# Kernel optimization log

Measured on AMD Instinct MI355X. Metric: run time of the kernel, lower is better.

## Reference

```python
import jax, jax.numpy as jnp
import numpy as np

EMB = 768
HEADS = 8
HEAD_DIM = EMB // HEADS
SCALE = HEAD_DIM ** -0.5


def setup_inputs() -> dict:
    key = jax.random.key(0)
    ks = jax.random.split(key, 9)
    s = EMB ** -0.5
    return {
        "x": jax.random.normal(ks[0], (2, 4096, EMB), dtype=jnp.float32),
        "Wq": jax.random.normal(ks[1], (EMB, EMB), dtype=jnp.float32) * s,
        "bq": jax.random.normal(ks[2], (EMB,), dtype=jnp.float32) * 0.02,
        "Wk": jax.random.normal(ks[3], (EMB, EMB), dtype=jnp.float32) * s,
        "bk": jax.random.normal(ks[4], (EMB,), dtype=jnp.float32) * 0.02,
        "Wv": jax.random.normal(ks[5], (EMB, EMB), dtype=jnp.float32) * s,
        "bv": jax.random.normal(ks[6], (EMB,), dtype=jnp.float32) * 0.02,
        "Wo": jax.random.normal(ks[7], (EMB, EMB), dtype=jnp.float32) * s,
        "bo": jax.random.normal(ks[8], (EMB,), dtype=jnp.float32) * 0.02,
    }


def reference(x, Wq, bq, Wk, bk, Wv, bv, Wo, bo):
    b, n, _ = x.shape
    def split_heads(t):  # [b, n, emb] -> [b, h, n, d]
        return t.reshape(b, n, HEADS, HEAD_DIM).transpose(0, 2, 1, 3)
    q = split_heads(x @ Wq + bq)
    k = split_heads(x @ Wk + bk)
    v = split_heads(x @ Wv + bv)
    scores = jnp.einsum('bhqd,bhkd->bhqk', q, k)
    # NOTE: faithful to source — softmax first, THEN multiply by scale.
    attn = jax.nn.softmax(scores, axis=-1) * SCALE
    out = jnp.einsum('bhqk,bhkd->bhqd', attn, v)
    out = out.transpose(0, 2, 1, 3).reshape(b, n, EMB)
    return out @ Wo + bo
```

## Files before the change

kernel.cpp:

```cpp
#include <hip/hip_runtime.h>
#include <hip/hip_fp16.h>


typedef _Float16 half8 __attribute__((ext_vector_type(8)));
typedef _Float16 half4 __attribute__((ext_vector_type(4)));
typedef float   float4_ __attribute__((ext_vector_type(4)));
typedef float   f32x16 __attribute__((ext_vector_type(16)));

#define SCALE 0.102062072615966f
#define LOG2E 1.44269504088896340736f

__device__ __forceinline__ float4_ mfma16(half8 a, half8 b, float4_ c) {
    return __builtin_amdgcn_mfma_f32_16x16x32_f16(a, b, c, 0, 0, 0);
}
__device__ __forceinline__ f32x16 mfma32(half8 a, half8 b, f32x16 c) {
    return __builtin_amdgcn_mfma_f32_32x32x16_f16(a, b, c, 0, 0, 0);
}
__device__ __forceinline__ void gload16(const _Float16* g, _Float16* l) {
    __builtin_amdgcn_global_load_lds(
        (const __attribute__((address_space(1))) void*)g,
        (__attribute__((address_space(3))) void*)l, 16, 0, 0);
}


__global__ void cast_x(const float* __restrict__ x, _Float16* __restrict__ xb) {
    int i = blockIdx.x * 256 + threadIdx.x;
    float4_ v = ((const float4_*)x)[i];
    half4 h = { (_Float16)v[0], (_Float16)v[1], (_Float16)v[2], (_Float16)v[3] };
    ((half4*)xb)[i] = h;
}

__global__ void prep_w(const float* __restrict__ Wq, const float* __restrict__ Wk,
                       const float* __restrict__ Wv, const float* __restrict__ Wo,
                       _Float16* __restrict__ wqkv, _Float16* __restrict__ wot) {
    __shared__ float tile[64][65];
    const int bid = blockIdx.x;
    const int mat = bid / 144, rem = bid % 144;
    const int kt = rem / 12, ct = rem % 12;
    const float* W = (mat == 0) ? Wq : (mat == 1) ? Wk : (mat == 2) ? Wv : Wo;
    const int k0 = kt * 64, c0 = ct * 64;
    const int t = threadIdx.x;
    const int lr = t >> 4, lc = (t & 15) * 4;
    #pragma unroll
    for (int i = 0; i < 4; ++i) {
        float4_ v = *(const float4_*)(W + (size_t)(k0 + i * 16 + lr) * 768 + c0 + lc);
        tile[i * 16 + lr][lc + 0] = v[0];
        tile[i * 16 + lr][lc + 1] = v[1];
        tile[i * 16 + lr][lc + 2] = v[2];
        tile[i * 16 + lr][lc + 3] = v[3];
    }
    __syncthreads();
    const int cr = t >> 2, kq = (t & 3) * 16;
    _Float16* dst = (mat < 3) ? (wqkv + ((size_t)(mat * 768 + c0 + cr)) * 768 + k0 + kq)
                              : (wot  + ((size_t)(c0 + cr)) * 768 + k0 + kq);
    half8 h0, h1;
    #pragma unroll
    for (int j = 0; j < 8; ++j) {
        h0[j] = (_Float16)tile[kq + j][cr];
        h1[j] = (_Float16)tile[kq + 8 + j][cr];
    }
    *(half8*)dst = h0;
    *(half8*)(dst + 8) = h1;
}

__global__ void prep_bias(const float* __restrict__ bq, const float* __restrict__ bk,
                          const float* __restrict__ bv, float* __restrict__ bqkv) {
    int i = blockIdx.x * 256 + threadIdx.x;
    float v = (i < 768) ? bq[i] : (i < 1536) ? bk[i - 768] : bv[i - 1536];
    bqkv[i] = v;
}

__global__ __launch_bounds__(256, 2) void gemm_kernel(
    const _Float16* __restrict__ A, const _Float16* __restrict__ Bt,
    const float* __restrict__ bias, int mode,
    _Float16* __restrict__ Qo, _Float16* __restrict__ Ko, _Float16* __restrict__ Vto,
    float* __restrict__ out)
{
    __shared__ alignas(16) _Float16 Af[16 * 512];
    __shared__ alignas(16) _Float16 Bf[16 * 512];
    const int tid = threadIdx.x;
    const int lane = tid & 63, w = tid >> 6;
    const int wm = w >> 1, wn = w & 1;
    const int l15 = lane & 15, l4 = lane >> 4;
    const int m0 = blockIdx.y * 128;
    const int n0 = blockIdx.x * 128;

    const _Float16* gs[8];
    _Float16* ld[8];
    #pragma unroll
    for (int i = 0; i < 8; ++i) {
        int f = (w & 1) * 8 + i;
        int rg = f >> 1, kc = f & 1;
        int r0 = ((w < 2) ? m0 : n0) + rg * 16;
        gs[i] = ((w < 2) ? A : Bt) + (size_t)(r0 + l15) * 768 + kc * 32 + l4 * 8;
        ld[i] = ((w < 2) ? Af : Bf) + f * 512;
    }

    float4_ acc[4][4] = {};

    for (int k0 = 0; k0 < 768; k0 += 64) {
        #pragma unroll
        for (int i = 0; i < 8; ++i)
            gload16(gs[i] + k0, ld[i]);
        __syncthreads();
        #pragma unroll
        for (int kc = 0; kc < 2; ++kc) {
            half8 bfr[4];
            #pragma unroll
            for (int nt = 0; nt < 4; ++nt)
                bfr[nt] = *(const half8*)(Bf + (size_t)(((wn * 4 + nt) * 2 + kc) * 512 + lane * 8));
            #pragma unroll
            for (int mt = 0; mt < 4; ++mt) {
                half8 afr = *(const half8*)(Af + (size_t)(((wm * 4 + mt) * 2 + kc) * 512 + lane * 8));
                #pragma unroll
                for (int nt = 0; nt < 4; ++nt)
                    acc[mt][nt] = mfma16(afr, bfr[nt], acc[mt][nt]);
            }
        }
        __syncthreads();
    }

    #pragma unroll
    for (int mt = 0; mt < 4; ++mt)
    #pragma unroll
    for (int nt = 0; nt < 4; ++nt) {
        int gc = n0 + wn * 64 + nt * 16 + l15;
        float bv_ = bias[gc];
        #pragma unroll
        for (int r = 0; r < 4; ++r) {
            int gm = m0 + wm * 64 + mt * 16 + l4 * 4 + r;
            float val = acc[mt][nt][r] + bv_;
            if (mode == 1) {
                out[(size_t)gm * 768 + gc] = val;
            } else {
                int b = gm >> 12, n = gm & 4095;
                if (gc < 768) {
                    int h = gc / 96, d = gc % 96;
                    Qo[(((size_t)(b * 8 + h)) * 4096 + n) * 96 + d] = (_Float16)(val * LOG2E);
                } else if (gc < 1536) {
                    int c = gc - 768, h = c / 96, d = c % 96;
                    int bh = b * 8 + h;
                    size_t idx = (((size_t)bh * 128 + (n >> 5)) * 6 + (d >> 4)) * 512
                               + (size_t)((d >> 3) & 1) * 256 + (size_t)(n & 31) * 8 + (d & 7);
                    Ko[idx] = (_Float16)val;
                } else {
                    int c = gc - 1536, h = c / 96, d = c % 96;
                    int bh = b * 8 + h;
                    size_t idx = (((size_t)bh * 64 + (n >> 6)) * 12 + ((n >> 4) & 3) * 3 + (d >> 5)) * 512
                               + (size_t)((n >> 3) & 1) * 256 + (size_t)(d & 31) * 8 + (n & 7);
                    Vto[idx] = (_Float16)val;
                }
            }
        }
    }
}

__global__ __launch_bounds__(256, 2) void attn_kernel(
    const _Float16* __restrict__ Q, const _Float16* __restrict__ Kf,
    const _Float16* __restrict__ Vf, _Float16* __restrict__ AO)
{
    __shared__ alignas(16) _Float16 kvbuf[2][24 * 512];
    __shared__ float tab[4][32];

    const int tid = threadIdx.x;
    const int lane = tid & 63, w = tid >> 6;
    const int l31 = lane & 31, hi = lane >> 5;

    const int B = blockIdx.x;
    const int xcd = B & 7, j = B >> 3;
    const int bh = 2 * xcd + (j >> 5);
    const int qb = j & 31;
    const int q0 = qb * 128 + w * 32;

    const size_t qBase = (size_t)bh * 4096 * 96;
    const _Float16* kfb = Kf + (size_t)bh * 393216;
    const _Float16* vfb = Vf + (size_t)bh * 393216;

    half8 qf[6];
    #pragma unroll
    for (int dch = 0; dch < 6; ++dch)
        qf[dch] = *(const half8*)(Q + qBase + (size_t)(q0 + l31) * 96 + dch * 16 + hi * 8);

    f32x16 o0 = {}, o1 = {}, o2 = {};
    float m = -1e30f, l = 0.f;

    const int fbase = w * 6;
    const _Float16* gbase = ((fbase < 12) ? (kfb + (size_t)fbase * 512)
                                          : (vfb + (size_t)(fbase - 12) * 512)) + lane * 8;

    #pragma unroll
    for (int i = 0; i < 6; ++i)
        gload16(gbase + i * 512, &kvbuf[0][(fbase + i) * 512]);
    __syncthreads();

    int cur = 0;
    for (int t = 0; t < 64; ++t) {
        const int tn = (t + 1) & 63;
        #pragma unroll
        for (int i = 0; i < 6; ++i)
            gload16(gbase + (size_t)tn * 6144 + i * 512, &kvbuf[cur ^ 1][(fbase + i) * 512]);

        const _Float16* kb = &kvbuf[cur][0];
        const _Float16* vb = &kvbuf[cur][12 * 512];

        f32x16 s0 = {}, s1 = {};
        __builtin_amdgcn_s_setprio(1);
        #pragma unroll
        for (int dch = 0; dch < 6; ++dch) {
            half8 k0 = *(const half8*)(kb + dch * 512 + lane * 8);
            half8 k1 = *(const half8*)(kb + (6 + dch) * 512 + lane * 8);
            s0 = mfma32(k0, qf[dch], s0);
            s1 = mfma32(k1, qf[dch], s1);
        }
        __builtin_amdgcn_s_setprio(0);

        float lm = fmaxf(s0[0], s0[1]);
        #pragma unroll
        for (int r = 2; r < 16; ++r) lm = fmaxf(lm, s0[r]);
        #pragma unroll
        for (int r = 0; r < 16; ++r) lm = fmaxf(lm, s1[r]);
        float pmax = fmaxf(lm, __shfl_xor(lm, 32));
        if (__any(pmax > m + 8.0f)) {
            float mn = fmaxf(m, pmax);
            float al = __builtin_exp2f(m - mn);
            m = mn; l *= al;
            if (hi == 0) tab[w][l31] = al;
            asm volatile("s_waitcnt lgkmcnt(0)" ::: "memory");
            #pragma unroll
            for (int r = 0; r < 16; ++r) {
                float alr = tab[w][(r & 3) + 8 * (r >> 2) + 4 * hi];
                o0[r] *= alr; o1[r] *= alr; o2[r] *= alr;
            }
        }
        float ls = 0.f;
        uint32_t Lp[16];
        #pragma unroll
        for (int kg = 0; kg < 2; ++kg) {
            const f32x16& s = kg ? s1 : s0;
            #pragma unroll
            for (int jg = 0; jg < 4; ++jg) {
                float p0 = __builtin_exp2f(s[4 * jg + 0] - m);
                float p1 = __builtin_exp2f(s[4 * jg + 1] - m);
                float p2 = __builtin_exp2f(s[4 * jg + 2] - m);
                float p3 = __builtin_exp2f(s[4 * jg + 3] - m);
                ls += (p0 + p1) + (p2 + p3);
                union { _Float16 h[2]; uint32_t u; } pk0, pk1;
                pk0.h[0] = (_Float16)p0; pk0.h[1] = (_Float16)p1;
                pk1.h[0] = (_Float16)p2; pk1.h[1] = (_Float16)p3;
                Lp[kg * 8 + jg * 2] = pk0.u; Lp[kg * 8 + jg * 2 + 1] = pk1.u;
            }
        }
        l += ls + __shfl_xor(ls, 32);

        half8 pa[4];
        #pragma unroll
        for (int kk = 0; kk < 4; ++kk) {
            uint32_t u0 = Lp[4 * kk], u1 = Lp[4 * kk + 1];
            uint32_t u2 = Lp[4 * kk + 2], u3 = Lp[4 * kk + 3];
            asm("v_permlane32_swap_b32 %0, %1" : "+v"(u0), "+v"(u2));
            asm("v_permlane32_swap_b32 %0, %1" : "+v"(u1), "+v"(u3));
            union { half8 h; uint32_t u[4]; } fr;
            fr.u[0] = u0; fr.u[1] = u1; fr.u[2] = u2; fr.u[3] = u3;
            pa[kk] = fr.h;
        }

        __builtin_amdgcn_s_setprio(1);
        #pragma unroll
        for (int kk = 0; kk < 4; ++kk) {
            half8 v0 = *(const half8*)(vb + (kk * 3 + 0) * 512 + lane * 8);
            half8 v1 = *(const half8*)(vb + (kk * 3 + 1) * 512 + lane * 8);
            half8 v2 = *(const half8*)(vb + (kk * 3 + 2) * 512 + lane * 8);
            o0 = mfma32(pa[kk], v0, o0);
            o1 = mfma32(pa[kk], v1, o1);
            o2 = mfma32(pa[kk], v2, o2);
        }
        __builtin_amdgcn_s_setprio(0);

        __syncthreads();
        cur ^= 1;
    }

    if (hi == 0) tab[w][l31] = l;
    asm volatile("s_waitcnt lgkmcnt(0)" ::: "memory");
    const int b = bh >> 3, h = bh & 7;
    #pragma unroll
    for (int r = 0; r < 16; ++r) {
        int qrow = (r & 3) + 8 * (r >> 2) + 4 * hi;
        float inv = SCALE / tab[w][qrow];
        int n = q0 + qrow;
        size_t base = ((size_t)(b * 4096 + n)) * 768 + h * 96 + l31;
        AO[base]      = (_Float16)(o0[r] * inv);
        AO[base + 32] = (_Float16)(o1[r] * inv);
        AO[base + 64] = (_Float16)(o2[r] * inv);
    }
}


extern "C" void kernel_launch(void* const* d_in, const int* in_sizes, int n_in,
                              void* d_out, int out_size, void* d_ws, size_t ws_size,
                              hipStream_t stream) {
    const float* x  = (const float*)d_in[0];
    const float* Wq = (const float*)d_in[1];
    const float* bq = (const float*)d_in[2];
    const float* Wk = (const float*)d_in[3];
    const float* bk = (const float*)d_in[4];
    const float* Wv = (const float*)d_in[5];
    const float* bv = (const float*)d_in[6];
    const float* Wo = (const float*)d_in[7];
    const float* bo = (const float*)d_in[8];
    float* out = (float*)d_out;

    char* ws = (char*)d_ws;
    _Float16* xb   = (_Float16*)(ws);
    _Float16* wqkv = (_Float16*)(ws + 12582912);
    _Float16* wot  = (_Float16*)(ws + 16121856);
    float*    bqkv = (float*)   (ws + 17301504);
    _Float16* Qb   = (_Float16*)(ws + 17310720);
    _Float16* Kfb  = (_Float16*)(ws + 29893632);
    _Float16* Vfb  = (_Float16*)(ws + 42476544);
    _Float16* AO   = xb;

    cast_x<<<6144, 256, 0, stream>>>(x, xb);
    prep_w<<<576, 256, 0, stream>>>(Wq, Wk, Wv, Wo, wqkv, wot);
    prep_bias<<<9, 256, 0, stream>>>(bq, bk, bv, bqkv);

    gemm_kernel<<<dim3(18, 64), 256, 0, stream>>>(xb, wqkv, bqkv, 0, Qb, Kfb, Vfb, nullptr);

    attn_kernel<<<512, 256, 0, stream>>>(Qb, Kfb, Vfb, AO);

    gemm_kernel<<<dim3(6, 64), 256, 0, stream>>>(AO, wot, bo, 1, nullptr, nullptr, nullptr, out);
}
```

Measured before the change: 280.2 us.

## Stage K/V tiles through registers instead of direct global-to-LDS loads

Replaces the asynchronous global_load_lds prefetch with ordinary global loads into registers, which are written to the other LDS buffer after the PV matmul, behind an extra barrier. It also replaces the permlane32 swaps with shfl_xor plus selects, restructures the row-max reduction into a tree, and lowers the rescale threshold from 8 to 6. The register staging adds 24 VGPRs, a second __syncthreads per tile and extra LDS store instructions. The shuffle path is likely more costly than the native permlane swap.

```diff
diff --git a/kernel.cpp b/kernel.cpp
--- a/kernel.cpp
+++ b/kernel.cpp
@@ -159,7 +159,7 @@
     const _Float16* __restrict__ Q, const _Float16* __restrict__ Kf,
     const _Float16* __restrict__ Vf, _Float16* __restrict__ AO)
 {
-    __shared__ alignas(16) _Float16 kvbuf[2][24 * 512];
+    __shared__ alignas(16) _Float16 lds[2][24 * 512];
     __shared__ float tab[4][32];
 
     const int tid = threadIdx.x;
@@ -185,45 +185,58 @@
     float m = -1e30f, l = 0.f;
 
     const int fbase = w * 6;
-    const _Float16* gbase = ((fbase < 12) ? (kfb + (size_t)fbase * 512)
-                                          : (vfb + (size_t)(fbase - 12) * 512)) + lane * 8;
-
+    half8 streg[6];
+
+    #pragma unroll
+    for (int i = 0; i < 6; ++i) {
+        int f = fbase + i;
+        const _Float16* g = (f < 12 ? kfb + (size_t)f * 512
+                                    : vfb + (size_t)(f - 12) * 512) + lane * 8;
+        streg[i] = *(const half8*)g;
+    }
     #pragma unroll
     for (int i = 0; i < 6; ++i)
-        gload16(gbase + i * 512, &kvbuf[0][(fbase + i) * 512]);
+        *(half8*)(&lds[0][(fbase + i) * 512 + lane * 8]) = streg[i];
     __syncthreads();
 
     int cur = 0;
     for (int t = 0; t < 64; ++t) {
         const int tn = (t + 1) & 63;
         #pragma unroll
-        for (int i = 0; i < 6; ++i)
-            gload16(gbase + (size_t)tn * 6144 + i * 512, &kvbuf[cur ^ 1][(fbase + i) * 512]);
-
-        const _Float16* kb = &kvbuf[cur][0];
-        const _Float16* vb = &kvbuf[cur][12 * 512];
+        for (int i = 0; i < 6; ++i) {
+            int f = fbase + i;
+            const _Float16* g = (f < 12 ? kfb + ((size_t)tn * 12 + f) * 512
+                                        : vfb + ((size_t)tn * 12 + (f - 12)) * 512) + lane * 8;
+            streg[i] = *(const half8*)g;
+        }
+
+        const _Float16* kb = &lds[cur][0];
+        const _Float16* vb = &lds[cur][12 * 512];
 
         f32x16 s0 = {}, s1 = {};
         __builtin_amdgcn_s_setprio(1);
         #pragma unroll
         for (int dch = 0; dch < 6; ++dch) {
-            half8 k0 = *(const half8*)(kb + dch * 512 + lane * 8);
-            half8 k1 = *(const half8*)(kb + (6 + dch) * 512 + lane * 8);
+            half8 k0 = *(const half8*)(kb + (0 * 6 + dch) * 512 + lane * 8);
+            half8 k1 = *(const half8*)(kb + (1 * 6 + dch) * 512 + lane * 8);
             s0 = mfma32(k0, qf[dch], s0);
             s1 = mfma32(k1, qf[dch], s1);
         }
         __builtin_amdgcn_s_setprio(0);
 
-        float lm = fmaxf(s0[0], s0[1]);
-        #pragma unroll
-        for (int r = 2; r < 16; ++r) lm = fmaxf(lm, s0[r]);
-        #pragma unroll
-        for (int r = 0; r < 16; ++r) lm = fmaxf(lm, s1[r]);
+        float mx[8];
+        #pragma unroll
+        for (int r = 0; r < 8; ++r)
+            mx[r] = fmaxf(fmaxf(s0[r], s0[r + 8]), fmaxf(s1[r], s1[r + 8]));
+        mx[0] = fmaxf(mx[0], mx[4]); mx[1] = fmaxf(mx[1], mx[5]);
+        mx[2] = fmaxf(mx[2], mx[6]); mx[3] = fmaxf(mx[3], mx[7]);
+        float lm = fmaxf(fmaxf(mx[0], mx[1]), fmaxf(mx[2], mx[3]));
         float pmax = fmaxf(lm, __shfl_xor(lm, 32));
-        if (__any(pmax > m + 8.0f)) {
+        if (__any(pmax > m + 6.0f)) {
             float mn = fmaxf(m, pmax);
             float al = __builtin_exp2f(m - mn);
-            m = mn; l *= al;
+            m = mn;
+            l *= al;
             if (hi == 0) tab[w][l31] = al;
             asm volatile("s_waitcnt lgkmcnt(0)" ::: "memory");
             #pragma unroll
@@ -233,35 +246,55 @@
             }
         }
         float ls = 0.f;
-        uint32_t Lp[16];
-        #pragma unroll
-        for (int kg = 0; kg < 2; ++kg) {
-            const f32x16& s = kg ? s1 : s0;
-            #pragma unroll
-            for (int jg = 0; jg < 4; ++jg) {
-                float p0 = __builtin_exp2f(s[4 * jg + 0] - m);
-                float p1 = __builtin_exp2f(s[4 * jg + 1] - m);
-                float p2 = __builtin_exp2f(s[4 * jg + 2] - m);
-                float p3 = __builtin_exp2f(s[4 * jg + 3] - m);
-                ls += (p0 + p1) + (p2 + p3);
-                union { _Float16 h[2]; uint32_t u; } pk0, pk1;
-                pk0.h[0] = (_Float16)p0; pk0.h[1] = (_Float16)p1;
-                pk1.h[0] = (_Float16)p2; pk1.h[1] = (_Float16)p3;
-                Lp[kg * 8 + jg * 2] = pk0.u; Lp[kg * 8 + jg * 2 + 1] = pk1.u;
-            }
+        uint32_t Lp0[8], Lp1[8];
+        #pragma unroll
+        for (int jg = 0; jg < 4; ++jg) {
+            float p0 = __builtin_exp2f(s0[4 * jg + 0] - m);
+            float p1 = __builtin_exp2f(s0[4 * jg + 1] - m);
+            float p2 = __builtin_exp2f(s0[4 * jg + 2] - m);
+            float p3 = __builtin_exp2f(s0[4 * jg + 3] - m);
+            ls += (p0 + p1) + (p2 + p3);
+            union { _Float16 h[2]; uint32_t u; } a, b2;
+            a.h[0] = (_Float16)p0; a.h[1] = (_Float16)p1;
+            b2.h[0] = (_Float16)p2; b2.h[1] = (_Float16)p3;
+            Lp0[jg * 2] = a.u; Lp0[jg * 2 + 1] = b2.u;
+        }
+        #pragma unroll
+        for (int jg = 0; jg < 4; ++jg) {
+            float p0 = __builtin_exp2f(s1[4 * jg + 0] - m);
+            float p1 = __builtin_exp2f(s1[4 * jg + 1] - m);
+            float p2 = __builtin_exp2f(s1[4 * jg + 2] - m);
+            float p3 = __builtin_exp2f(s1[4 * jg + 3] - m);
+            ls += (p0 + p1) + (p2 + p3);
+            union { _Float16 h[2]; uint32_t u; } a, b2;
+            a.h[0] = (_Float16)p0; a.h[1] = (_Float16)p1;
+            b2.h[0] = (_Float16)p2; b2.h[1] = (_Float16)p3;
+            Lp1[jg * 2] = a.u; Lp1[jg * 2 + 1] = b2.u;
         }
         l += ls + __shfl_xor(ls, 32);
 
         half8 pa[4];
         #pragma unroll
-        for (int kk = 0; kk < 4; ++kk) {
-            uint32_t u0 = Lp[4 * kk], u1 = Lp[4 * kk + 1];
-            uint32_t u2 = Lp[4 * kk + 2], u3 = Lp[4 * kk + 3];
-            asm("v_permlane32_swap_b32 %0, %1" : "+v"(u0), "+v"(u2));
-            asm("v_permlane32_swap_b32 %0, %1" : "+v"(u1), "+v"(u3));
+        for (int kc = 0; kc < 2; ++kc) {
+            uint32_t a0 = Lp0[4 * kc], a1 = Lp0[4 * kc + 1];
+            uint32_t a2 = Lp0[4 * kc + 2], a3 = Lp0[4 * kc + 3];
+            uint32_t w0 = __shfl_xor((int)a0, 32), w1 = __shfl_xor((int)a1, 32);
+            uint32_t w2 = __shfl_xor((int)a2, 32), w3 = __shfl_xor((int)a3, 32);
             union { half8 h; uint32_t u[4]; } fr;
-            fr.u[0] = u0; fr.u[1] = u1; fr.u[2] = u2; fr.u[3] = u3;
-            pa[kk] = fr.h;
+            fr.u[0] = hi ? w2 : a0;  fr.u[1] = hi ? w3 : a1;
+            fr.u[2] = hi ? a2 : w0;  fr.u[3] = hi ? a3 : w1;
+            pa[kc] = fr.h;
+        }
+        #pragma unroll
+        for (int kc = 0; kc < 2; ++kc) {
+            uint32_t a0 = Lp1[4 * kc], a1 = Lp1[4 * kc + 1];
+            uint32_t a2 = Lp1[4 * kc + 2], a3 = Lp1[4 * kc + 3];
+            uint32_t w0 = __shfl_xor((int)a0, 32), w1 = __shfl_xor((int)a1, 32);
+            uint32_t w2 = __shfl_xor((int)a2, 32), w3 = __shfl_xor((int)a3, 32);
+            union { half8 h; uint32_t u[4]; } fr;
+            fr.u[0] = hi ? w2 : a0;  fr.u[1] = hi ? w3 : a1;
+            fr.u[2] = hi ? a2 : w0;  fr.u[3] = hi ? a3 : w1;
+            pa[2 + kc] = fr.h;
         }
 
         __builtin_amdgcn_s_setprio(1);
@@ -276,6 +309,10 @@
         }
         __builtin_amdgcn_s_setprio(0);
 
+        __syncthreads();
+        #pragma unroll
+        for (int i = 0; i < 6; ++i)
+            *(half8*)(&lds[cur ^ 1][(fbase + i) * 512 + lane * 8]) = streg[i];
         __syncthreads();
         cur ^= 1;
     }
```

Result: slower. 290.6 us (+3.7%).
